# Kernel tuning notes

Hardware: AMD Instinct MI355X
Metric: run time of the kernel (lower is better)

## Reference

```python
import jax, jax.numpy as jnp
import numpy as np

L = 3            # frequency bands
WIN = 8          # window side
N = WIN * WIN    # tokens per window (64)
HEADS = 8
DIM = 512
HEAD_DIM = DIM // HEADS
SCALE = HEAD_DIM ** -0.5
BNW = 512        # number of windows (per-band batch)
B_ = L * BNW     # leading batch of x


def _rel_index():
    # relative_position_index buffer from the torch module, shape (N, N)
    coords = np.stack(np.meshgrid(np.arange(WIN), np.arange(WIN), indexing='ij'))
    flat = coords.reshape(2, -1)                             # (2, N)
    rel = (flat[:, :, None] - flat[:, None, :]).transpose(1, 2, 0).astype(np.int64)
    rel[..., 0] += WIN - 1
    rel[..., 1] += WIN - 1
    rel[..., 0] *= 2 * WIN - 1
    return rel.sum(-1)                                       # (N, N), values in [0, 225)


def _mask_freq():
    # type='intra': 0 on diagonal L-blocks, -100 off-diagonal
    m = np.where(np.eye(L, dtype=bool), 0.0, -100.0).astype(np.float32)
    return np.kron(m, np.ones((N, N), dtype=np.float32))     # (L*N, L*N)


REL_IDX = jnp.asarray(_rel_index())
MASK_FREQ = jnp.asarray(_mask_freq())


def setup_inputs() -> dict:
    key = jax.random.key(0)
    ks = jax.random.split(key, 8)
    s = 0.02
    return {
        'x': jax.random.normal(ks[0], (B_, N, DIM), dtype=jnp.float32),
        'Wq': s * jax.random.normal(ks[1], (DIM, DIM), dtype=jnp.float32),
        'bq': jnp.zeros((DIM,), dtype=jnp.float32),
        'Wkv': s * jax.random.normal(ks[2], (DIM, 2 * DIM), dtype=jnp.float32),
        'bkv': jnp.zeros((2 * DIM,), dtype=jnp.float32),
        'bias_tables': s * jax.random.normal(ks[3], (L * L, (2 * WIN - 1) ** 2, HEADS), dtype=jnp.float32),
        'Wp': s * jax.random.normal(ks[4], (DIM, DIM), dtype=jnp.float32),
        'bp': jnp.zeros((DIM,), dtype=jnp.float32),
    }


def reference(x, Wq, bq, Wkv, bkv, bias_tables, Wp, bp):
    Bt, Nt, C = x.shape  # (L*BNW, N, DIM)
    # linear qkv projection -> (B_, H, N, d)
    q = (x @ Wq + bq).reshape(Bt, Nt, HEADS, HEAD_DIM).transpose(0, 2, 1, 3)
    kv = (x @ Wkv + bkv).reshape(Bt, Nt, 2, HEADS, HEAD_DIM)
    k = kv[:, :, 0].transpose(0, 2, 1, 3)
    v = kv[:, :, 1].transpose(0, 2, 1, 3)

    def regroup(t):  # (L*BNW, H, N, d) -> (BNW, H, L*N, d)
        return t.reshape(L, BNW, HEADS, Nt, HEAD_DIM).transpose(1, 2, 0, 3, 4).reshape(BNW, HEADS, L * Nt, HEAD_DIM)

    q = regroup(q) * SCALE
    k = regroup(k)
    v = regroup(v)

    attn = jnp.einsum('bhqd,bhkd->bhqk', q, k)  # (BNW, H, L*N, L*N)

    # per-band-pair relative position bias gather: (9, N*N, H) -> (H, L*N, L*N)
    bias = bias_tables[:, REL_IDX.reshape(-1), :]
    bias = bias.reshape(L, L, Nt, Nt, HEADS).transpose(4, 0, 2, 1, 3).reshape(HEADS, L * Nt, L * Nt)

    attn = attn + bias[None] + MASK_FREQ[None, None]
    attn = jax.nn.softmax(attn, axis=-1)

    out = jnp.einsum('bhqk,bhkd->bhqd', attn, v)  # (BNW, H, L*N, d)
    # (BNW,H,(L N),d) -> ((L BNW), N, H*d)
    out = out.reshape(BNW, HEADS, L, Nt, HEAD_DIM).transpose(2, 0, 3, 1, 4).reshape(Bt, Nt, C)
    return out @ Wp + bp
```

## Files before the change

### kernel.cpp

```cpp
#include <hip/hip_runtime.h>
#include <stdint.h>

typedef __bf16 bf16x8 __attribute__((ext_vector_type(8)));
typedef float f32x4 __attribute__((ext_vector_type(4)));

#define SCALE_Q 0.125f

__device__ __forceinline__ unsigned short f2bf(float f) {
  unsigned int u = __float_as_uint(f);
  u = (u + 0x7fffu + ((u >> 16) & 1u)) >> 16;
  return (unsigned short)u;
}

__device__ __forceinline__ void gl_lds16(const unsigned short* g, unsigned short* l) {
  __builtin_amdgcn_global_load_lds(
      (const __attribute__((address_space(1))) unsigned int*)g,
      (__attribute__((address_space(3))) unsigned int*)l, 16, 0, 0);
}

__device__ __forceinline__ f32x4 mfma16(bf16x8 a, bf16x8 b, f32x4 c) {
  return __builtin_amdgcn_mfma_f32_16x16x32_bf16(a, b, c, 0, 0, 0);
}

__global__ void convert_x_kernel(const float* __restrict__ x, unsigned short* __restrict__ xb) {
  int i = blockIdx.x * 256 + threadIdx.x;
  float4 f = ((const float4*)x)[i];
  ushort4 o;
  o.x = f2bf(f.x); o.y = f2bf(f.y); o.z = f2bf(f.z); o.w = f2bf(f.w);
  ((ushort4*)xb)[i] = o;
}

__global__ void prep_w_kernel(const float* __restrict__ Wq, const float* __restrict__ Wkv,
                              const float* __restrict__ bq, const float* __restrict__ bkv,
                              const float* __restrict__ Wp,
                              unsigned short* __restrict__ wt_all,
                              unsigned short* __restrict__ wpt,
                              float* __restrict__ b_all) {
  int i = blockIdx.x * 256 + threadIdx.x;
  const int N1 = 1536 * 512;
  const int N2 = N1 + 512 * 512;
  const int N3 = N2 + 1536;
  if (i < N1) {
    int n = i >> 9, k = i & 511;
    float v = (n < 512) ? Wq[k * 512 + n] : Wkv[k * 1024 + (n - 512)];
    wt_all[n * 512 + k] = f2bf(v);
  } else if (i < N2) {
    int j = i - N1; int n = j >> 9, k = j & 511;
    wpt[n * 512 + k] = f2bf(Wp[k * 512 + n]);
  } else if (i < N3) {
    int n = i - N2;
    b_all[n] = (n < 512) ? bq[n] : bkv[n - 512];
  }
}

template <int MODE>
__global__ __launch_bounds__(256) void gemm_kernel(
    const unsigned short* __restrict__ A, const unsigned short* __restrict__ Bt,
    const float* __restrict__ bias,
    unsigned short* __restrict__ qb, unsigned short* __restrict__ kb,
    unsigned short* __restrict__ vtb, float* __restrict__ outf) {
  __shared__ __align__(16) unsigned short lds_a[128 * 32];
  __shared__ __align__(16) unsigned short lds_b[128 * 32];
  const int tid = threadIdx.x;
  const int m0 = blockIdx.x * 128;
  const int n0 = blockIdx.y * 128;
  const int lane = tid & 63;
  const int wv = tid >> 6;
  const int wm = (wv >> 1) * 64, wn = (wv & 1) * 64;
  const int quad = lane >> 4, li = lane & 15;
  const int srow = tid >> 2, sq = (tid & 3) * 8;

  const unsigned short* ga = A + (size_t)(m0 + srow) * 512 + sq;
  const unsigned short* gb = Bt + (size_t)(n0 + srow) * 512 + sq;
  unsigned short* la = lds_a + wv * 512;
  unsigned short* lb = lds_b + wv * 512;

  f32x4 acc[4][4];
#pragma unroll
  for (int i = 0; i < 4; i++)
#pragma unroll
    for (int j = 0; j < 4; j++) acc[i][j] = {0.f, 0.f, 0.f, 0.f};

  for (int k0 = 0; k0 < 512; k0 += 32) {
    gl_lds16(ga + k0, la);
    gl_lds16(ga + 64 * 512 + k0, la + 2048);
    gl_lds16(gb + k0, lb);
    gl_lds16(gb + 64 * 512 + k0, lb + 2048);
    __syncthreads();
    bf16x8 af[4], bfr[4];
#pragma unroll
    for (int i = 0; i < 4; i++)
      af[i] = *(const bf16x8*)&lds_a[(wm + i * 16 + li) * 32 + quad * 8];
#pragma unroll
    for (int j = 0; j < 4; j++)
      bfr[j] = *(const bf16x8*)&lds_b[(wn + j * 16 + li) * 32 + quad * 8];
#pragma unroll
    for (int i = 0; i < 4; i++)
#pragma unroll
      for (int j = 0; j < 4; j++)
        acc[i][j] = mfma16(af[i], bfr[j], acc[i][j]);
    __syncthreads();
  }

#pragma unroll
  for (int j = 0; j < 4; j++) {
    const int c = n0 + wn + j * 16 + li;
    const float badd = bias[c];
#pragma unroll
    for (int i = 0; i < 4; i++) {
      const int mb = m0 + wm + i * 16 + quad * 4;
#pragma unroll
      for (int r = 0; r < 4; r++) {
        const int m = mb + r;
        float v = acc[i][j][r] + badd;
        if (MODE == 1) {
          outf[(size_t)m * 512 + c] = v;
        } else {
          const int b = m >> 6, nn = m & 63;
          const int l = b >> 9, w = b & 511;
          const int seq = l * 64 + nn;
          const int d = c & 63;
          if (c < 512) {
            const int h = c >> 6;
            qb[((size_t)((w * 8 + h) * 192 + seq)) * 64 + d] = f2bf(v * SCALE_Q);
          } else if (c < 1024) {
            const int h = (c - 512) >> 6;
            kb[((size_t)((w * 8 + h) * 192 + seq)) * 64 + d] = f2bf(v);
          } else {
            const int h = (c - 1024) >> 6;
            vtb[((size_t)((w * 8 + h) * 64 + d)) * 192 + seq] = f2bf(v);
          }
        }
      }
    }
  }
}

__global__ __launch_bounds__(256) void attn_kernel(
    const unsigned short* __restrict__ qb, const unsigned short* __restrict__ kb,
    const unsigned short* __restrict__ vtb, const float* __restrict__ bias_tables,
    unsigned short* __restrict__ ab) {
  const int w = blockIdx.x, h = blockIdx.y, lq = blockIdx.z;
  __shared__ float bias_l[3 * 225];
  __shared__ __align__(16) unsigned short lds_p[64 * 200];

  const int tid = threadIdx.x;
  for (int t = tid; t < 675; t += 256) {
    int lk = t / 225, rel = t - lk * 225;
    bias_l[t] = bias_tables[((lq * 3 + lk) * 225 + rel) * 8 + h];
  }
  __syncthreads();

  const int lane = tid & 63, wv = tid >> 6;
  const int quad = lane >> 4, li = lane & 15;
  const size_t base_qk = (size_t)(w * 8 + h) * 192 * 64;

  const int qrow = lq * 64 + wv * 16 + li;
  bf16x8 aq0 = *(const bf16x8*)&qb[base_qk + (size_t)qrow * 64 + quad * 8];
  bf16x8 aq1 = *(const bf16x8*)&qb[base_qk + (size_t)qrow * 64 + 32 + quad * 8];

  f32x4 s[12];
#pragma unroll
  for (int nt = 0; nt < 12; nt++) {
    const int krow = nt * 16 + li;
    bf16x8 bk0 = *(const bf16x8*)&kb[base_qk + (size_t)krow * 64 + quad * 8];
    bf16x8 bk1 = *(const bf16x8*)&kb[base_qk + (size_t)krow * 64 + 32 + quad * 8];
    f32x4 a = {0.f, 0.f, 0.f, 0.f};
    a = mfma16(aq0, bk0, a);
    a = mfma16(aq1, bk1, a);
    s[nt] = a;
  }

#pragma unroll
  for (int nt = 0; nt < 12; nt++) {
    const int lk = nt >> 2;
    const int jj = (nt * 16 + li) & 63;
    const int yj = jj >> 3, xj = jj & 7;
    const float mask = (lk == lq) ? 0.f : -100.f;
#pragma unroll
    for (int r = 0; r < 4; r++) {
      const int i = wv * 16 + quad * 4 + r;
      const int yi = i >> 3, xi = i & 7;
      const int rel = (yi - yj + 7) * 15 + (xi - xj + 7);
      s[nt][r] += bias_l[lk * 225 + rel] + mask;
    }
  }

#pragma unroll
  for (int r = 0; r < 4; r++) {
    float m = -1e30f;
#pragma unroll
    for (int nt = 0; nt < 12; nt++) m = fmaxf(m, s[nt][r]);
#pragma unroll
    for (int off = 1; off < 16; off <<= 1) m = fmaxf(m, __shfl_xor(m, off, 64));
    float sum = 0.f;
#pragma unroll
    for (int nt = 0; nt < 12; nt++) { float e = __expf(s[nt][r] - m); s[nt][r] = e; sum += e; }
#pragma unroll
    for (int off = 1; off < 16; off <<= 1) sum += __shfl_xor(sum, off, 64);
    const float inv = 1.f / sum;
#pragma unroll
    for (int nt = 0; nt < 12; nt++) s[nt][r] *= inv;
  }

#pragma unroll
  for (int nt = 0; nt < 12; nt++)
#pragma unroll
    for (int r = 0; r < 4; r++)
      lds_p[(wv * 16 + quad * 4 + r) * 200 + nt * 16 + li] = f2bf(s[nt][r]);
  __syncthreads();

  const size_t base_v = (size_t)(w * 8 + h) * 64 * 192;
  f32x4 o[4];
#pragma unroll
  for (int nt = 0; nt < 4; nt++) o[nt] = {0.f, 0.f, 0.f, 0.f};
#pragma unroll
  for (int ks = 0; ks < 6; ks++) {
    bf16x8 ap = *(const bf16x8*)&lds_p[(wv * 16 + li) * 200 + ks * 32 + quad * 8];
#pragma unroll
    for (int nt = 0; nt < 4; nt++) {
      bf16x8 bv = *(const bf16x8*)&vtb[base_v + (size_t)(nt * 16 + li) * 192 + ks * 32 + quad * 8];
      o[nt] = mfma16(ap, bv, o[nt]);
    }
  }

  const size_t mg_base = (size_t)(lq * 512 + w) * 64;
#pragma unroll
  for (int nt = 0; nt < 4; nt++) {
    const int col = h * 64 + nt * 16 + li;
#pragma unroll
    for (int r = 0; r < 4; r++) {
      const int i = wv * 16 + quad * 4 + r;
      ab[(mg_base + i) * 512 + col] = f2bf(o[nt][r]);
    }
  }
}

extern "C" void kernel_launch(void* const* d_in, const int* in_sizes, int n_in,
                              void* d_out, int out_size, void* d_ws, size_t ws_size,
                              hipStream_t stream) {
  const float* x    = (const float*)d_in[0];
  const float* Wq   = (const float*)d_in[1];
  const float* bq   = (const float*)d_in[2];
  const float* Wkv  = (const float*)d_in[3];
  const float* bkv  = (const float*)d_in[4];
  const float* bt   = (const float*)d_in[5];
  const float* Wp   = (const float*)d_in[6];
  const float* bp   = (const float*)d_in[7];
  float* out = (float*)d_out;

  const long long SZ = 100663296LL;
  char* ws = (char*)d_ws;
  unsigned short* xb     = (unsigned short*)(ws);
  unsigned short* qb     = (unsigned short*)(ws + 1 * SZ);
  unsigned short* kb     = (unsigned short*)(ws + 2 * SZ);
  unsigned short* vtb    = (unsigned short*)(ws + 3 * SZ);
  unsigned short* ab     = (unsigned short*)(ws + 4 * SZ);
  unsigned short* wt_all = (unsigned short*)(ws + 5 * SZ);
  unsigned short* wpt    = (unsigned short*)(ws + 5 * SZ + 1572864);
  float*          b_all  = (float*)(ws + 5 * SZ + 1572864 + 524288);

  convert_x_kernel<<<49152, 256, 0, stream>>>(x, xb);
  prep_w_kernel<<<4102, 256, 0, stream>>>(Wq, Wkv, bq, bkv, Wp, wt_all, wpt, b_all);
  gemm_kernel<0><<<dim3(768, 12), 256, 0, stream>>>(xb, wt_all, b_all, qb, kb, vtb, nullptr);
  attn_kernel<<<dim3(512, 8, 3), 256, 0, stream>>>(qb, kb, vtb, bt, ab);
  gemm_kernel<1><<<dim3(768, 4), 256, 0, stream>>>(ab, wpt, bp, nullptr, nullptr, nullptr, out);
}
```

Measured before the change: 1.100 ms.

## Skip masked cross-band attention blocks and double-buffer GEMM LDS tiles

The attention kernel now computes scores, softmax and P·V only over the query's own frequency band. The off-diagonal band blocks carry a -100 mask, so their softmax weights are around e^-100 and can be dropped. This cuts the QK, softmax and PV work and the bias staging to a third, at the cost of a tiny numerical difference from the reference. Separately, the projection GEMM double-buffers its LDS tiles so the next K-slice's global-to-LDS load is issued while the current slice's MFMAs run.

```diff
diff --git a/kernel.cpp b/kernel.cpp
--- a/kernel.cpp
+++ b/kernel.cpp
@@ -59,8 +59,8 @@
     const float* __restrict__ bias,
     unsigned short* __restrict__ qb, unsigned short* __restrict__ kb,
     unsigned short* __restrict__ vtb, float* __restrict__ outf) {
-  __shared__ __align__(16) unsigned short lds_a[128 * 32];
-  __shared__ __align__(16) unsigned short lds_b[128 * 32];
+  __shared__ __align__(16) unsigned short lds_a[2][128 * 32];
+  __shared__ __align__(16) unsigned short lds_b[2][128 * 32];
   const int tid = threadIdx.x;
   const int m0 = blockIdx.x * 128;
   const int n0 = blockIdx.y * 128;
@@ -72,8 +72,6 @@
 
   const unsigned short* ga = A + (size_t)(m0 + srow) * 512 + sq;
   const unsigned short* gb = Bt + (size_t)(n0 + srow) * 512 + sq;
-  unsigned short* la = lds_a + wv * 512;
-  unsigned short* lb = lds_b + wv * 512;
 
   f32x4 acc[4][4];
 #pragma unroll
@@ -81,19 +79,35 @@
 #pragma unroll
     for (int j = 0; j < 4; j++) acc[i][j] = {0.f, 0.f, 0.f, 0.f};
 
-  for (int k0 = 0; k0 < 512; k0 += 32) {
-    gl_lds16(ga + k0, la);
-    gl_lds16(ga + 64 * 512 + k0, la + 2048);
-    gl_lds16(gb + k0, lb);
-    gl_lds16(gb + 64 * 512 + k0, lb + 2048);
-    __syncthreads();
+  {
+    unsigned short* la = &lds_a[0][wv * 512];
+    unsigned short* lb = &lds_b[0][wv * 512];
+    gl_lds16(ga, la);
+    gl_lds16(ga + 64 * 512, la + 2048);
+    gl_lds16(gb, lb);
+    gl_lds16(gb + 64 * 512, lb + 2048);
+  }
+  __syncthreads();
+
+#pragma unroll
+  for (int kk = 0; kk < 16; kk++) {
+    const int cur = kk & 1;
+    if (kk < 15) {
+      const int k1 = (kk + 1) * 32;
+      unsigned short* la = &lds_a[cur ^ 1][wv * 512];
+      unsigned short* lb = &lds_b[cur ^ 1][wv * 512];
+      gl_lds16(ga + k1, la);
+      gl_lds16(ga + 64 * 512 + k1, la + 2048);
+      gl_lds16(gb + k1, lb);
+      gl_lds16(gb + 64 * 512 + k1, lb + 2048);
+    }
     bf16x8 af[4], bfr[4];
 #pragma unroll
     for (int i = 0; i < 4; i++)
-      af[i] = *(const bf16x8*)&lds_a[(wm + i * 16 + li) * 32 + quad * 8];
+      af[i] = *(const bf16x8*)&lds_a[cur][(wm + i * 16 + li) * 32 + quad * 8];
 #pragma unroll
     for (int j = 0; j < 4; j++)
-      bfr[j] = *(const bf16x8*)&lds_b[(wn + j * 16 + li) * 32 + quad * 8];
+      bfr[j] = *(const bf16x8*)&lds_b[cur][(wn + j * 16 + li) * 32 + quad * 8];
 #pragma unroll
     for (int i = 0; i < 4; i++)
 #pragma unroll
@@ -141,14 +155,11 @@
     const unsigned short* __restrict__ vtb, const float* __restrict__ bias_tables,
     unsigned short* __restrict__ ab) {
   const int w = blockIdx.x, h = blockIdx.y, lq = blockIdx.z;
-  __shared__ float bias_l[3 * 225];
-  __shared__ __align__(16) unsigned short lds_p[64 * 200];
+  __shared__ float bias_l[225];
+  __shared__ __align__(16) unsigned short lds_p[64 * 72];
 
   const int tid = threadIdx.x;
-  for (int t = tid; t < 675; t += 256) {
-    int lk = t / 225, rel = t - lk * 225;
-    bias_l[t] = bias_tables[((lq * 3 + lk) * 225 + rel) * 8 + h];
-  }
+  if (tid < 225) bias_l[tid] = bias_tables[((lq * 3 + lq) * 225 + tid) * 8 + h];
   __syncthreads();
 
   const int lane = tid & 63, wv = tid >> 6;
@@ -159,10 +170,10 @@
   bf16x8 aq0 = *(const bf16x8*)&qb[base_qk + (size_t)qrow * 64 + quad * 8];
   bf16x8 aq1 = *(const bf16x8*)&qb[base_qk + (size_t)qrow * 64 + 32 + quad * 8];
 
-  f32x4 s[12];
-#pragma unroll
-  for (int nt = 0; nt < 12; nt++) {
-    const int krow = nt * 16 + li;
+  f32x4 s[4];
+#pragma unroll
+  for (int nt = 0; nt < 4; nt++) {
+    const int krow = lq * 64 + nt * 16 + li;
     bf16x8 bk0 = *(const bf16x8*)&kb[base_qk + (size_t)krow * 64 + quad * 8];
     bf16x8 bk1 = *(const bf16x8*)&kb[base_qk + (size_t)krow * 64 + 32 + quad * 8];
     f32x4 a = {0.f, 0.f, 0.f, 0.f};
@@ -172,17 +183,15 @@
   }
 
 #pragma unroll
-  for (int nt = 0; nt < 12; nt++) {
-    const int lk = nt >> 2;
-    const int jj = (nt * 16 + li) & 63;
+  for (int nt = 0; nt < 4; nt++) {
+    const int jj = nt * 16 + li;
     const int yj = jj >> 3, xj = jj & 7;
-    const float mask = (lk == lq) ? 0.f : -100.f;
 #pragma unroll
     for (int r = 0; r < 4; r++) {
       const int i = wv * 16 + quad * 4 + r;
       const int yi = i >> 3, xi = i & 7;
       const int rel = (yi - yj + 7) * 15 + (xi - xj + 7);
-      s[nt][r] += bias_l[lk * 225 + rel] + mask;
+      s[nt][r] += bias_l[rel];
     }
   }
 
@@ -190,24 +199,24 @@
   for (int r = 0; r < 4; r++) {
     float m = -1e30f;
 #pragma unroll
-    for (int nt = 0; nt < 12; nt++) m = fmaxf(m, s[nt][r]);
+    for (int nt = 0; nt < 4; nt++) m = fmaxf(m, s[nt][r]);
 #pragma unroll
     for (int off = 1; off < 16; off <<= 1) m = fmaxf(m, __shfl_xor(m, off, 64));
     float sum = 0.f;
 #pragma unroll
-    for (int nt = 0; nt < 12; nt++) { float e = __expf(s[nt][r] - m); s[nt][r] = e; sum += e; }
+    for (int nt = 0; nt < 4; nt++) { float e = __expf(s[nt][r] - m); s[nt][r] = e; sum += e; }
 #pragma unroll
     for (int off = 1; off < 16; off <<= 1) sum += __shfl_xor(sum, off, 64);
     const float inv = 1.f / sum;
 #pragma unroll
-    for (int nt = 0; nt < 12; nt++) s[nt][r] *= inv;
-  }
-
-#pragma unroll
-  for (int nt = 0; nt < 12; nt++)
+    for (int nt = 0; nt < 4; nt++) s[nt][r] *= inv;
+  }
+
+#pragma unroll
+  for (int nt = 0; nt < 4; nt++)
 #pragma unroll
     for (int r = 0; r < 4; r++)
-      lds_p[(wv * 16 + quad * 4 + r) * 200 + nt * 16 + li] = f2bf(s[nt][r]);
+      lds_p[(wv * 16 + quad * 4 + r) * 72 + nt * 16 + li] = f2bf(s[nt][r]);
   __syncthreads();
 
   const size_t base_v = (size_t)(w * 8 + h) * 64 * 192;
@@ -215,11 +224,11 @@
 #pragma unroll
   for (int nt = 0; nt < 4; nt++) o[nt] = {0.f, 0.f, 0.f, 0.f};
 #pragma unroll
-  for (int ks = 0; ks < 6; ks++) {
-    bf16x8 ap = *(const bf16x8*)&lds_p[(wv * 16 + li) * 200 + ks * 32 + quad * 8];
+  for (int ks = 0; ks < 2; ks++) {
+    bf16x8 ap = *(const bf16x8*)&lds_p[(wv * 16 + li) * 72 + ks * 32 + quad * 8];
 #pragma unroll
     for (int nt = 0; nt < 4; nt++) {
-      bf16x8 bv = *(const bf16x8*)&vtb[base_v + (size_t)(nt * 16 + li) * 192 + ks * 32 + quad * 8];
+      bf16x8 bv = *(const bf16x8*)&vtb[base_v + (size_t)(nt * 16 + li) * 192 + lq * 64 + ks * 32 + quad * 8];
       o[nt] = mfma16(ap, bv, o[nt]);
     }
   }
```

After: 900.0 us. -18.2%, faster.
